# Kernel tuning notes

Hardware: AMD Instinct MI355X
Metric: run time of the kernel (lower is better)

## Reference

```python
import jax, jax.numpy as jnp
import numpy as np

N_GEN, N_LOAD, N_OR, N_EX = 10000, 20000, 35000, 35000
N = N_GEN + N_LOAD + N_OR + N_EX  # 100000 objects
E = 1_600_000                      # edges (avg degree 16)
H = 64                             # N_node_hidden
L_HID = 7                          # N_GCN_layers - 1
NEG = 0.1                          # LeakyReLU negative slope
WS = 0.05                          # weight scale


def setup_inputs() -> dict:
    key = jax.random.key(0)
    ks = jax.random.split(key, 32)
    f = lambda i, s: jax.random.normal(ks[i], s, jnp.float32)
    p = lambda i, s: WS * jax.random.normal(ks[i], s, jnp.float32)
    return {
        "x_gen": f(0, (N_GEN, 3)),
        "x_load": f(1, (N_LOAD, 3)),
        "x_or": f(2, (N_OR, 6)),
        "x_ex": f(3, (N_EX, 6)),
        "edge_index": jax.random.randint(ks[4], (2, E), 0, N, jnp.int32),
        "object_ptv": jnp.arange(N, dtype=jnp.int32),
        "W_gen1": p(5, (3, H)), "b_gen1": p(6, (H,)),
        "W_gen2": p(7, (H, H)), "b_gen2": p(8, (H,)),
        "W_load1": p(9, (3, H)), "b_load1": p(10, (H,)),
        "W_load2": p(11, (H, H)), "b_load2": p(12, (H,)),
        "W_or1": p(13, (6, H)), "b_or1": p(14, (H,)),
        "W_or2": p(15, (H, H)), "b_or2": p(16, (H,)),
        "W_ex1": p(17, (6, H)), "b_ex1": p(18, (H,)),
        "W_ex2": p(19, (H, H)), "b_ex2": p(20, (H,)),
        "Wl_h": p(21, (L_HID, H, H)),
        "Wr_h": p(22, (L_HID, H, H)),
        "b_h": p(23, (L_HID, H)),
        "Wl_last": p(24, (H, 1)),
        "Wr_last": p(25, (H, 1)),
        "b_last": p(26, (1,)),
    }


def _encode(x, W1, b1, W2, b2):
    h = jax.nn.leaky_relu(x @ W1 + b1, NEG)
    return jax.nn.leaky_relu(h @ W2 + b2, NEG)


def reference(x_gen, x_load, x_or, x_ex, edge_index, object_ptv,
              W_gen1, b_gen1, W_gen2, b_gen2,
              W_load1, b_load1, W_load2, b_load2,
              W_or1, b_or1, W_or2, b_or2,
              W_ex1, b_ex1, W_ex2, b_ex2,
              Wl_h, Wr_h, b_h, Wl_last, Wr_last, b_last):
    # per-object-type MLP encoders
    xg = _encode(x_gen, W_gen1, b_gen1, W_gen2, b_gen2)
    xl = _encode(x_load, W_load1, b_load1, W_load2, b_load2)
    xo = _encode(x_or, W_or1, b_or1, W_or2, b_or2)
    xe = _encode(x_ex, W_ex1, b_ex1, W_ex2, b_ex2)
    x = jnp.concatenate([xg, xl, xo, xe], axis=0)[object_ptv]  # [N, H]

    src, dst = edge_index[0], edge_index[1]

    def sage(h, Wl, Wr, b):
        # SAGEConv(aggr='add', root_weight=True): lin_l(sum_j h_j) + lin_r(h_i) + b
        agg = jax.ops.segment_sum(h[src], dst, num_segments=N)  # gather + scatter-add
        return agg @ Wl + h @ Wr + b

    def step(h, params):
        Wl, Wr, b = params
        return jax.nn.leaky_relu(sage(h, Wl, Wr, b), NEG), None

    x, _ = jax.lax.scan(step, x, (Wl_h, Wr_h, b_h))
    return jax.nn.sigmoid(sage(x, Wl_last, Wr_last, b_last))  # [N, 1]
```

## Files before the change

### kernel.cpp

```cpp
#include <hip/hip_runtime.h>
#include <math.h>

#define HD 64
#define NEGS 0.1f
#define CHUNK 2048
#define NPART 8
#define QMAX 440.0f
#define QEPS 1e-30f

typedef unsigned int u32;
typedef unsigned char u8;
typedef float f32x2 __attribute__((ext_vector_type(2)));

__device__ __forceinline__ float leaky(float v) { return v > 0.f ? v : NEGS * v; }

__device__ __forceinline__ u32 pk4(float a, float b, float c, float d) {
    u32 r = __builtin_amdgcn_cvt_pk_fp8_f32(a, b, 0, false);
    r = __builtin_amdgcn_cvt_pk_fp8_f32(c, d, r, true);
    return r;
}

__global__ void zero_i32(int* __restrict__ p, int n) {
    int i = blockIdx.x * blockDim.x + threadIdx.x;
    int stride = gridDim.x * blockDim.x;
    for (; i < n; i += stride) p[i] = 0;
}

template <int IN>
__global__ void encode_k(const float* __restrict__ x,
                         const float* __restrict__ W1, const float* __restrict__ b1,
                         const float* __restrict__ W2, const float* __restrict__ b2,
                         u8* __restrict__ out, float* __restrict__ outS, int n) {
    __shared__ float sW2[HD * HD];
    for (int idx = threadIdx.x; idx < HD * HD; idx += blockDim.x) sW2[idx] = W2[idx];
    __syncthreads();
    int wave = threadIdx.x >> 6, lane = threadIdx.x & 63;
    int i = blockIdx.x * 4 + wave;
    if (i >= n) return;
    float h1 = b1[lane];
#pragma unroll
    for (int d = 0; d < IN; ++d) h1 += x[i * IN + d] * W1[d * HD + lane];
    h1 = leaky(h1);
    float h2 = b2[lane];
#pragma unroll
    for (int k = 0; k < HD; ++k) {
        float hk = __shfl(h1, k);
        h2 += hk * sW2[k * HD + lane];
    }
    float val = leaky(h2);
    float am = fabsf(val);
#pragma unroll
    for (int off = 32; off > 0; off >>= 1) am = fmaxf(am, __shfl_xor(am, off));
    float qs, recip;
    if (am < QEPS) { qs = 0.f; recip = 0.f; }
    else { qs = QMAX / am; recip = am / QMAX; }
    float sv = val * qs;
    float v1 = __shfl_down(sv, 1);
    float v2 = __shfl_down(sv, 2);
    float v3 = __shfl_down(sv, 3);
    if ((lane & 3) == 0)
        ((u32*)(out + (size_t)i * HD))[lane >> 2] = pk4(sv, v1, v2, v3);
    if (lane == 0) outS[i] = recip;
}

__global__ void gather_f8(const u8* __restrict__ enc, const float* __restrict__ encS,
                          const int* __restrict__ ptv,
                          u8* __restrict__ out, float* __restrict__ outS, int n) {
    int idx = blockIdx.x * blockDim.x + threadIdx.x;
    int stride = gridDim.x * blockDim.x;
    int total = n * 4;
    for (; idx < total; idx += stride) {
        int i = idx >> 2, ch = idx & 3;
        int p = ptv[i];
        ((uint4*)(out + (size_t)i * HD))[ch] =
            ((const uint4*)(enc + (size_t)p * HD))[ch];
        if (ch == 0) outS[i] = encS[p];
    }
}

__global__ void __launch_bounds__(256) hist_part(const int* __restrict__ dst,
                                                 int* __restrict__ counts,
                                                 int E_, int part_sz) {
    int part = blockIdx.x & (NPART - 1);
    int slice = blockIdx.x >> 3;
    int nslices = gridDim.x >> 3;
    int lo = part * part_sz, hi = lo + part_sz;
    for (int e = slice * blockDim.x + threadIdx.x; e < E_; e += nslices * blockDim.x) {
        int d = dst[e];
        if (d >= lo && d < hi) atomicAdd(&counts[d], 1);
    }
}

__global__ void scan1(const int* __restrict__ counts, int* __restrict__ bsum, int n) {
    __shared__ int s[256];
    int b = blockIdx.x, t = threadIdx.x;
    int base = b * CHUNK + t * 8;
    int sum = 0;
#pragma unroll
    for (int u = 0; u < 8; ++u) {
        int i = base + u;
        if (i < n) sum += counts[i];
    }
    s[t] = sum;
    __syncthreads();
    for (int off = 128; off > 0; off >>= 1) {
        if (t < off) s[t] += s[t + off];
        __syncthreads();
    }
    if (t == 0) bsum[b] = s[0];
}

__global__ void scan2(int* __restrict__ bsum, int nb, int* __restrict__ row_ptr, int n) {
    if (threadIdx.x == 0 && blockIdx.x == 0) {
        int run = 0;
        for (int b = 0; b < nb; ++b) {
            int v = bsum[b];
            bsum[b] = run;
            run += v;
        }
        row_ptr[n] = run;
    }
}

__global__ void scan3(const int* __restrict__ counts, const int* __restrict__ bsum,
                      int* __restrict__ row_ptr, int* __restrict__ pos, int n) {
    __shared__ int s[256];
    int b = blockIdx.x, t = threadIdx.x;
    int base = b * CHUNK + t * 8;
    int c[8];
    int sum = 0;
#pragma unroll
    for (int u = 0; u < 8; ++u) {
        int i = base + u;
        c[u] = (i < n) ? counts[i] : 0;
        sum += c[u];
    }
    s[t] = sum;
    __syncthreads();
    for (int off = 1; off < 256; off <<= 1) {
        int v = (t >= off) ? s[t - off] : 0;
        __syncthreads();
        s[t] += v;
        __syncthreads();
    }
    int run = bsum[b] + s[t] - sum;
#pragma unroll
    for (int u = 0; u < 8; ++u) {
        int i = base + u;
        if (i < n) {
            row_ptr[i] = run;
            pos[i] = run;
            run += c[u];
        }
    }
}

__global__ void __launch_bounds__(256) scatter_part(const int* __restrict__ src,
                                                    const int* __restrict__ dst,
                                                    int* __restrict__ pos,
                                                    int* __restrict__ col,
                                                    int E_, int part_sz) {
    int part = blockIdx.x & (NPART - 1);
    int slice = blockIdx.x >> 3;
    int nslices = gridDim.x >> 3;
    int lo = part * part_sz, hi = lo + part_sz;
    for (int e = slice * blockDim.x + threadIdx.x; e < E_; e += nslices * blockDim.x) {
        int d = dst[e];
        if (d >= lo && d < hi) {
            int p = atomicAdd(&pos[d], 1);
            col[p] = src[e];
        }
    }
}

__global__ void __launch_bounds__(256) agg_f8(const u8* __restrict__ hin,
                                              const float* __restrict__ hs,
                                              u8* __restrict__ agg,
                                              float* __restrict__ aggS,
                                              const int* __restrict__ row_ptr,
                                              const int* __restrict__ col, int n) {
    int wid = threadIdx.x >> 6, lane = threadIdx.x & 63;
    int g = lane >> 4, s = lane & 15;
    int wpb = blockDim.x >> 6;
    int stride = gridDim.x * wpb;
    for (int i = blockIdx.x * wpb + wid; i < n; i += stride) {
        int beg = row_ptr[i], end = row_ptr[i + 1];
        int deg = end - beg;
        float4 a0 = make_float4(0.f, 0.f, 0.f, 0.f);
        float4 a1 = make_float4(0.f, 0.f, 0.f, 0.f);
        float4 a2 = make_float4(0.f, 0.f, 0.f, 0.f);
        float4 a3 = make_float4(0.f, 0.f, 0.f, 0.f);
        for (int base = 0; base < deg; base += 64) {
            int m = deg - base;
            if (m > 64) m = 64;
            int cidx = (lane < m) ? col[beg + base + lane] : 0;
            int k = g;
            for (; k + 12 < m; k += 16) {
                int c0 = __shfl(cidx, k);
                int c1 = __shfl(cidx, k + 4);
                int c2 = __shfl(cidx, k + 8);
                int c3 = __shfl(cidx, k + 12);
                u32 v0 = ((const u32*)(hin + (size_t)c0 * HD))[s];
                u32 v1 = ((const u32*)(hin + (size_t)c1 * HD))[s];
                u32 v2 = ((const u32*)(hin + (size_t)c2 * HD))[s];
                u32 v3 = ((const u32*)(hin + (size_t)c3 * HD))[s];
                float s0 = hs[c0], s1 = hs[c1], s2 = hs[c2], s3 = hs[c3];
                f32x2 p0 = __builtin_amdgcn_cvt_pk_f32_fp8(v0, false);
                f32x2 q0 = __builtin_amdgcn_cvt_pk_f32_fp8(v0, true);
                f32x2 p1 = __builtin_amdgcn_cvt_pk_f32_fp8(v1, false);
                f32x2 q1 = __builtin_amdgcn_cvt_pk_f32_fp8(v1, true);
                f32x2 p2 = __builtin_amdgcn_cvt_pk_f32_fp8(v2, false);
                f32x2 q2 = __builtin_amdgcn_cvt_pk_f32_fp8(v2, true);
                f32x2 p3 = __builtin_amdgcn_cvt_pk_f32_fp8(v3, false);
                f32x2 q3 = __builtin_amdgcn_cvt_pk_f32_fp8(v3, true);
                a0.x = fmaf(p0.x, s0, a0.x); a0.y = fmaf(p0.y, s0, a0.y);
                a0.z = fmaf(q0.x, s0, a0.z); a0.w = fmaf(q0.y, s0, a0.w);
                a1.x = fmaf(p1.x, s1, a1.x); a1.y = fmaf(p1.y, s1, a1.y);
                a1.z = fmaf(q1.x, s1, a1.z); a1.w = fmaf(q1.y, s1, a1.w);
                a2.x = fmaf(p2.x, s2, a2.x); a2.y = fmaf(p2.y, s2, a2.y);
                a2.z = fmaf(q2.x, s2, a2.z); a2.w = fmaf(q2.y, s2, a2.w);
                a3.x = fmaf(p3.x, s3, a3.x); a3.y = fmaf(p3.y, s3, a3.y);
                a3.z = fmaf(q3.x, s3, a3.z); a3.w = fmaf(q3.y, s3, a3.w);
            }
            for (; k < m; k += 4) {
                int c0 = __shfl(cidx, k);
                u32 v0 = ((const u32*)(hin + (size_t)c0 * HD))[s];
                float s0 = hs[c0];
                f32x2 p0 = __builtin_amdgcn_cvt_pk_f32_fp8(v0, false);
                f32x2 q0 = __builtin_amdgcn_cvt_pk_f32_fp8(v0, true);
                a0.x = fmaf(p0.x, s0, a0.x); a0.y = fmaf(p0.y, s0, a0.y);
                a0.z = fmaf(q0.x, s0, a0.z); a0.w = fmaf(q0.y, s0, a0.w);
            }
        }
        a0.x += a1.x + a2.x + a3.x;
        a0.y += a1.y + a2.y + a3.y;
        a0.z += a1.z + a2.z + a3.z;
        a0.w += a1.w + a2.w + a3.w;
        a0.x += __shfl_xor(a0.x, 16);
        a0.y += __shfl_xor(a0.y, 16);
        a0.z += __shfl_xor(a0.z, 16);
        a0.w += __shfl_xor(a0.w, 16);
        a0.x += __shfl_xor(a0.x, 32);
        a0.y += __shfl_xor(a0.y, 32);
        a0.z += __shfl_xor(a0.z, 32);
        a0.w += __shfl_xor(a0.w, 32);
        float am = fmaxf(fmaxf(fabsf(a0.x), fabsf(a0.y)),
                         fmaxf(fabsf(a0.z), fabsf(a0.w)));
        am = fmaxf(am, __shfl_xor(am, 1));
        am = fmaxf(am, __shfl_xor(am, 2));
        am = fmaxf(am, __shfl_xor(am, 4));
        am = fmaxf(am, __shfl_xor(am, 8));
        float qs, recip;
        if (am < QEPS) { qs = 0.f; recip = 0.f; }
        else { qs = QMAX / am; recip = am / QMAX; }
        if (g == 0) {
            ((u32*)(agg + (size_t)i * HD))[s] =
                pk4(a0.x * qs, a0.y * qs, a0.z * qs, a0.w * qs);
            if (s == 0) aggS[i] = recip;
        }
    }
}

__global__ void __launch_bounds__(256) sage_gemm_f8(const u8* __restrict__ agg,
                                                    const float* __restrict__ aggS,
                                                    const u8* __restrict__ h,
                                                    const float* __restrict__ hS,
                                                    u8* __restrict__ hout,
                                                    float* __restrict__ houtS,
                                                    const float* __restrict__ Wl,
                                                    const float* __restrict__ Wr,
                                                    const float* __restrict__ bias, int n) {
    __shared__ float Ws[128][64];
    __shared__ float Xs[64][132];
    int tid = threadIdx.x;
    for (int idx = tid; idx < 64 * 64; idx += 256) {
        int k = idx >> 6, j = idx & 63;
        Ws[k][j] = Wl[idx];
        Ws[64 + k][j] = Wr[idx];
    }
    int tcol = tid & 15, trow = tid >> 4;
    int j0 = tcol * 4;
    float b0 = bias[j0], b1 = bias[j0 + 1], b2 = bias[j0 + 2], b3 = bias[j0 + 3];
    int ntiles = (n + 63) >> 6;
    for (int t = blockIdx.x; t < ntiles; t += gridDim.x) {
        int base = t << 6;
        __syncthreads();
#pragma unroll
        for (int u = 0; u < 4; ++u) {
            int idx = tid + u * 256;
            int row = idx >> 4, ch = idx & 15;
            int grow = base + row;
            uint2 q = make_uint2(0u, 0u);
            float sc = 0.f;
            if (grow < n) {
                q = (ch < 8) ? ((const uint2*)(agg + (size_t)grow * HD))[ch]
                             : ((const uint2*)(h + (size_t)grow * HD))[ch - 8];
                sc = (ch < 8) ? aggS[grow] : hS[grow];
            }
            f32x2 p0 = __builtin_amdgcn_cvt_pk_f32_fp8(q.x, false);
            f32x2 p1 = __builtin_amdgcn_cvt_pk_f32_fp8(q.x, true);
            f32x2 p2 = __builtin_amdgcn_cvt_pk_f32_fp8(q.y, false);
            f32x2 p3 = __builtin_amdgcn_cvt_pk_f32_fp8(q.y, true);
            float* xp = &Xs[row][ch * 8];
            xp[0] = p0.x * sc; xp[1] = p0.y * sc; xp[2] = p1.x * sc; xp[3] = p1.y * sc;
            xp[4] = p2.x * sc; xp[5] = p2.y * sc; xp[6] = p3.x * sc; xp[7] = p3.y * sc;
        }
        __syncthreads();
        float acc[4][4];
#pragma unroll
        for (int r = 0; r < 4; ++r)
#pragma unroll
            for (int c = 0; c < 4; ++c) acc[r][c] = 0.f;
#pragma unroll 4
        for (int k4 = 0; k4 < 32; ++k4) {
            int k = k4 * 4;
            float4 x0 = *(const float4*)&Xs[trow][k];
            float4 x1 = *(const float4*)&Xs[trow + 16][k];
            float4 x2 = *(const float4*)&Xs[trow + 32][k];
            float4 x3 = *(const float4*)&Xs[trow + 48][k];
            float4 w0 = *(const float4*)&Ws[k][j0];
            float4 w1 = *(const float4*)&Ws[k + 1][j0];
            float4 w2 = *(const float4*)&Ws[k + 2][j0];
            float4 w3 = *(const float4*)&Ws[k + 3][j0];
            float4 xr[4] = {x0, x1, x2, x3};
#pragma unroll
            for (int r = 0; r < 4; ++r) {
                acc[r][0] += xr[r].x * w0.x + xr[r].y * w1.x + xr[r].z * w2.x + xr[r].w * w3.x;
                acc[r][1] += xr[r].x * w0.y + xr[r].y * w1.y + xr[r].z * w2.y + xr[r].w * w3.y;
                acc[r][2] += xr[r].x * w0.z + xr[r].y * w1.z + xr[r].z * w2.z + xr[r].w * w3.z;
                acc[r][3] += xr[r].x * w0.w + xr[r].y * w1.w + xr[r].z * w2.w + xr[r].w * w3.w;
            }
        }
#pragma unroll
        for (int r = 0; r < 4; ++r) {
            int grow = base + trow + 16 * r;
            float o0 = leaky(acc[r][0] + b0);
            float o1 = leaky(acc[r][1] + b1);
            float o2 = leaky(acc[r][2] + b2);
            float o3 = leaky(acc[r][3] + b3);
            float am = fmaxf(fmaxf(fabsf(o0), fabsf(o1)), fmaxf(fabsf(o2), fabsf(o3)));
            am = fmaxf(am, __shfl_xor(am, 1));
            am = fmaxf(am, __shfl_xor(am, 2));
            am = fmaxf(am, __shfl_xor(am, 4));
            am = fmaxf(am, __shfl_xor(am, 8));
            float qs, recip;
            if (am < QEPS) { qs = 0.f; recip = 0.f; }
            else { qs = QMAX / am; recip = am / QMAX; }
            if (grow < n) {
                ((u32*)(hout + (size_t)grow * HD))[tcol] =
                    pk4(o0 * qs, o1 * qs, o2 * qs, o3 * qs);
                if (tcol == 0) houtS[grow] = recip;
            }
        }
    }
}

__global__ void __launch_bounds__(256) dot_f8(const u8* __restrict__ h,
                                              const float* __restrict__ hS,
                                              const float* __restrict__ Wl,
                                              const float* __restrict__ Wr,
                                              float* __restrict__ sb, float* __restrict__ tb,
                                              int n) {
    int wid = threadIdx.x >> 6, lane = threadIdx.x & 63;
    float wl = Wl[lane], wr = Wr[lane];
    int wpb = blockDim.x >> 6;
    int stride = gridDim.x * wpb;
    for (int i = blockIdx.x * wpb + wid; i < n; i += stride) {
        u32 v = ((const u32*)(h + (size_t)i * HD))[lane >> 2];
        float sc = hS[i];
        f32x2 lo = __builtin_amdgcn_cvt_pk_f32_fp8(v, false);
        f32x2 hi = __builtin_amdgcn_cvt_pk_f32_fp8(v, true);
        float hv = ((lane & 2) ? ((lane & 1) ? hi.y : hi.x)
                               : ((lane & 1) ? lo.y : lo.x)) * sc;
        float a = hv * wl;
        float c = hv * wr;
#pragma unroll
        for (int off = 32; off > 0; off >>= 1) {
            a += __shfl_xor(a, off);
            c += __shfl_xor(c, off);
        }
        if (lane == 0) {
            sb[i] = a;
            tb[i] = c;
        }
    }
}

__global__ void __launch_bounds__(256) last_k(const float* __restrict__ sb,
                                              const float* __restrict__ tb,
                                              const int* __restrict__ row_ptr,
                                              const int* __restrict__ col,
                                              const float* __restrict__ b_last,
                                              float* __restrict__ out, int n) {
    float b0 = b_last[0];
    int stride = gridDim.x * blockDim.x;
    for (int i = blockIdx.x * blockDim.x + threadIdx.x; i < n; i += stride) {
        int beg = row_ptr[i], end = row_ptr[i + 1];
        float acc = 0.f;
        for (int k = beg; k < end; ++k) acc += sb[col[k]];
        out[i] = 1.f / (1.f + expf(-(acc + tb[i] + b0)));
    }
}

extern "C" void kernel_launch(void* const* d_in, const int* in_sizes, int n_in,
                              void* d_out, int out_size, void* d_ws, size_t ws_size,
                              hipStream_t stream) {
    const float* x_gen = (const float*)d_in[0];
    const float* x_load = (const float*)d_in[1];
    const float* x_or = (const float*)d_in[2];
    const float* x_ex = (const float*)d_in[3];
    const int* edge = (const int*)d_in[4];
    const int* ptv = (const int*)d_in[5];
    const float* W_gen1 = (const float*)d_in[6];
    const float* b_gen1 = (const float*)d_in[7];
    const float* W_gen2 = (const float*)d_in[8];
    const float* b_gen2 = (const float*)d_in[9];
    const float* W_load1 = (const float*)d_in[10];
    const float* b_load1 = (const float*)d_in[11];
    const float* W_load2 = (const float*)d_in[12];
    const float* b_load2 = (const float*)d_in[13];
    const float* W_or1 = (const float*)d_in[14];
    const float* b_or1 = (const float*)d_in[15];
    const float* W_or2 = (const float*)d_in[16];
    const float* b_or2 = (const float*)d_in[17];
    const float* W_ex1 = (const float*)d_in[18];
    const float* b_ex1 = (const float*)d_in[19];
    const float* W_ex2 = (const float*)d_in[20];
    const float* b_ex2 = (const float*)d_in[21];
    const float* Wl_h = (const float*)d_in[22];
    const float* Wr_h = (const float*)d_in[23];
    const float* b_h = (const float*)d_in[24];
    const float* Wl_last = (const float*)d_in[25];
    const float* Wr_last = (const float*)d_in[26];
    const float* b_last = (const float*)d_in[27];

    int n_gen = in_sizes[0] / 3;
    int n_load = in_sizes[1] / 3;
    int n_or = in_sizes[2] / 6;
    int n_ex = in_sizes[3] / 6;
    int E_ = in_sizes[4] / 2;
    int N_ = in_sizes[5];
    const int* srcv = edge;
    const int* dstv = edge + E_;

    char* ws = (char*)d_ws;
    size_t off = 0;
    auto alloc = [&](size_t bytes) -> void* {
        void* p = ws + off;
        off = (off + bytes + 255) & ~(size_t)255;
        return p;
    };
    u8* enc = (u8*)alloc((size_t)N_ * HD);
    float* encS = (float*)alloc((size_t)N_ * 4);
    u8* hA = (u8*)alloc((size_t)N_ * HD);
    float* sA = (float*)alloc((size_t)N_ * 4);
    u8* hB = (u8*)alloc((size_t)N_ * HD);
    float* sB = (float*)alloc((size_t)N_ * 4);
    int* counts = (int*)alloc((size_t)N_ * 4);
    int* row_ptr = (int*)alloc((size_t)(N_ + 1) * 4);
    int* pos = (int*)alloc((size_t)N_ * 4);
    int* bsum = (int*)alloc(256 * 4);
    int* csr_col = (int*)alloc((size_t)E_ * 4);
    float* sbuf = (float*)alloc((size_t)N_ * 4);
    float* tbuf = (float*)alloc((size_t)N_ * 4);
    u8* agg = enc;
    float* aggS = encS;
    (void)ws_size;

    int part_sz = (N_ + NPART - 1) / NPART;

    zero_i32<<<256, 256, 0, stream>>>(counts, N_);

    encode_k<3><<<(n_gen + 3) / 4, 256, 0, stream>>>(x_gen, W_gen1, b_gen1, W_gen2, b_gen2,
                                                     enc, encS, n_gen);
    encode_k<3><<<(n_load + 3) / 4, 256, 0, stream>>>(x_load, W_load1, b_load1, W_load2, b_load2,
                                                      enc + (size_t)n_gen * HD, encS + n_gen, n_load);
    encode_k<6><<<(n_or + 3) / 4, 256, 0, stream>>>(x_or, W_or1, b_or1, W_or2, b_or2,
                                                    enc + (size_t)(n_gen + n_load) * HD,
                                                    encS + n_gen + n_load, n_or);
    encode_k<6><<<(n_ex + 3) / 4, 256, 0, stream>>>(x_ex, W_ex1, b_ex1, W_ex2, b_ex2,
                                                    enc + (size_t)(n_gen + n_load + n_or) * HD,
                                                    encS + n_gen + n_load + n_or, n_ex);

    gather_f8<<<512, 256, 0, stream>>>(enc, encS, ptv, hA, sA, N_);

    hist_part<<<2048, 256, 0, stream>>>(dstv, counts, E_, part_sz);
    int nb = (N_ + CHUNK - 1) / CHUNK;
    scan1<<<nb, 256, 0, stream>>>(counts, bsum, N_);
    scan2<<<1, 64, 0, stream>>>(bsum, nb, row_ptr, N_);
    scan3<<<nb, 256, 0, stream>>>(counts, bsum, row_ptr, pos, N_);
    scatter_part<<<2048, 256, 0, stream>>>(srcv, dstv, pos, csr_col, E_, part_sz);

    int ntiles = (N_ + 63) >> 6;
    int ggrid = ntiles < 512 ? ntiles : 512;
    u8* cur = hA;   float* curS = sA;
    u8* nxt = hB;   float* nxtS = sB;
    for (int l = 0; l < 7; ++l) {
        agg_f8<<<4096, 256, 0, stream>>>(cur, curS, agg, aggS, row_ptr, csr_col, N_);
        sage_gemm_f8<<<ggrid, 256, 0, stream>>>(agg, aggS, cur, curS, nxt, nxtS,
                                                Wl_h + (size_t)l * HD * HD,
                                                Wr_h + (size_t)l * HD * HD,
                                                b_h + (size_t)l * HD, N_);
        u8* t = cur; cur = nxt; nxt = t;
        float* ts = curS; curS = nxtS; nxtS = ts;
    }
    dot_f8<<<1024, 256, 0, stream>>>(cur, curS, Wl_last, Wr_last, sbuf, tbuf, N_);
    last_k<<<512, 256, 0, stream>>>(sbuf, tbuf, row_ptr, csr_col, b_last,
                                    (float*)d_out, N_);
}
```

Baseline: 830.2 us.

## Assign one node per 16-lane group in fp8 aggregation kernel

The aggregation kernel now maps each destination node to a 16-lane quarter-wave group instead of a full 64-lane wavefront. Each group loads up to 16 neighbour indices at a time and walks its neighbours serially, which removes the cross-group shuffle reductions and the idle store lanes. With average degree 16, the old layout left most of each wavefront's lanes doing little work. The launch grid is resized to cover about 16 nodes per block. The tradeoff is lower memory-level parallelism per node, and more divergence when degrees differ between groups in the same wave.

```diff
diff --git a/kernel.cpp b/kernel.cpp
--- a/kernel.cpp
+++ b/kernel.cpp
@@ -179,32 +179,34 @@
                                               float* __restrict__ aggS,
                                               const int* __restrict__ row_ptr,
                                               const int* __restrict__ col, int n) {
-    int wid = threadIdx.x >> 6, lane = threadIdx.x & 63;
-    int g = lane >> 4, s = lane & 15;
-    int wpb = blockDim.x >> 6;
-    int stride = gridDim.x * wpb;
-    for (int i = blockIdx.x * wpb + wid; i < n; i += stride) {
+    int tid = threadIdx.x;
+    int g = (tid >> 4) & 3;
+    int s = tid & 15;
+    int gid = (blockIdx.x * blockDim.x + tid) >> 4;
+    int ngroups = (gridDim.x * blockDim.x) >> 4;
+    int gbase = g << 4;
+    for (int i = gid; i < n; i += ngroups) {
         int beg = row_ptr[i], end = row_ptr[i + 1];
         int deg = end - beg;
         float4 a0 = make_float4(0.f, 0.f, 0.f, 0.f);
         float4 a1 = make_float4(0.f, 0.f, 0.f, 0.f);
         float4 a2 = make_float4(0.f, 0.f, 0.f, 0.f);
         float4 a3 = make_float4(0.f, 0.f, 0.f, 0.f);
-        for (int base = 0; base < deg; base += 64) {
+        for (int base = 0; base < deg; base += 16) {
             int m = deg - base;
-            if (m > 64) m = 64;
-            int cidx = (lane < m) ? col[beg + base + lane] : 0;
-            int k = g;
-            for (; k + 12 < m; k += 16) {
-                int c0 = __shfl(cidx, k);
-                int c1 = __shfl(cidx, k + 4);
-                int c2 = __shfl(cidx, k + 8);
-                int c3 = __shfl(cidx, k + 12);
-                u32 v0 = ((const u32*)(hin + (size_t)c0 * HD))[s];
-                u32 v1 = ((const u32*)(hin + (size_t)c1 * HD))[s];
-                u32 v2 = ((const u32*)(hin + (size_t)c2 * HD))[s];
-                u32 v3 = ((const u32*)(hin + (size_t)c3 * HD))[s];
-                float s0 = hs[c0], s1 = hs[c1], s2 = hs[c2], s3 = hs[c3];
+            if (m > 16) m = 16;
+            int cidx = (s < m) ? col[beg + base + s] : 0;
+            int k = 0;
+            for (; k + 3 < m; k += 4) {
+                int r0 = __shfl(cidx, gbase + k);
+                int r1 = __shfl(cidx, gbase + k + 1);
+                int r2 = __shfl(cidx, gbase + k + 2);
+                int r3 = __shfl(cidx, gbase + k + 3);
+                u32 v0 = ((const u32*)(hin + (size_t)r0 * HD))[s];
+                u32 v1 = ((const u32*)(hin + (size_t)r1 * HD))[s];
+                u32 v2 = ((const u32*)(hin + (size_t)r2 * HD))[s];
+                u32 v3 = ((const u32*)(hin + (size_t)r3 * HD))[s];
+                float s0 = hs[r0], s1 = hs[r1], s2 = hs[r2], s3 = hs[r3];
                 f32x2 p0 = __builtin_amdgcn_cvt_pk_f32_fp8(v0, false);
                 f32x2 q0 = __builtin_amdgcn_cvt_pk_f32_fp8(v0, true);
                 f32x2 p1 = __builtin_amdgcn_cvt_pk_f32_fp8(v1, false);
@@ -222,10 +224,10 @@
                 a3.x = fmaf(p3.x, s3, a3.x); a3.y = fmaf(p3.y, s3, a3.y);
                 a3.z = fmaf(q3.x, s3, a3.z); a3.w = fmaf(q3.y, s3, a3.w);
             }
-            for (; k < m; k += 4) {
-                int c0 = __shfl(cidx, k);
-                u32 v0 = ((const u32*)(hin + (size_t)c0 * HD))[s];
-                float s0 = hs[c0];
+            for (; k < m; ++k) {
+                int r0 = __shfl(cidx, gbase + k);
+                u32 v0 = ((const u32*)(hin + (size_t)r0 * HD))[s];
+                float s0 = hs[r0];
                 f32x2 p0 = __builtin_amdgcn_cvt_pk_f32_fp8(v0, false);
                 f32x2 q0 = __builtin_amdgcn_cvt_pk_f32_fp8(v0, true);
                 a0.x = fmaf(p0.x, s0, a0.x); a0.y = fmaf(p0.y, s0, a0.y);
@@ -236,14 +238,6 @@
         a0.y += a1.y + a2.y + a3.y;
         a0.z += a1.z + a2.z + a3.z;
         a0.w += a1.w + a2.w + a3.w;
-        a0.x += __shfl_xor(a0.x, 16);
-        a0.y += __shfl_xor(a0.y, 16);
-        a0.z += __shfl_xor(a0.z, 16);
-        a0.w += __shfl_xor(a0.w, 16);
-        a0.x += __shfl_xor(a0.x, 32);
-        a0.y += __shfl_xor(a0.y, 32);
-        a0.z += __shfl_xor(a0.z, 32);
-        a0.w += __shfl_xor(a0.w, 32);
         float am = fmaxf(fmaxf(fabsf(a0.x), fabsf(a0.y)),
                          fmaxf(fabsf(a0.z), fabsf(a0.w)));
         am = fmaxf(am, __shfl_xor(am, 1));
@@ -253,11 +247,9 @@
         float qs, recip;
         if (am < QEPS) { qs = 0.f; recip = 0.f; }
         else { qs = QMAX / am; recip = am / QMAX; }
-        if (g == 0) {
-            ((u32*)(agg + (size_t)i * HD))[s] =
-                pk4(a0.x * qs, a0.y * qs, a0.z * qs, a0.w * qs);
-            if (s == 0) aggS[i] = recip;
-        }
+        ((u32*)(agg + (size_t)i * HD))[s] =
+            pk4(a0.x * qs, a0.y * qs, a0.z * qs, a0.w * qs);
+        if (s == 0) aggS[i] = recip;
     }
 }
 
@@ -493,10 +485,12 @@
 
     int ntiles = (N_ + 63) >> 6;
     int ggrid = ntiles < 512 ? ntiles : 512;
+    int agrid = (N_ + 15) / 16;
+    if (agrid > 6250) agrid = 6250;
     u8* cur = hA;   float* curS = sA;
     u8* nxt = hB;   float* nxtS = sB;
     for (int l = 0; l < 7; ++l) {
-        agg_f8<<<4096, 256, 0, stream>>>(cur, curS, agg, aggS, row_ptr, csr_col, N_);
+        agg_f8<<<agrid, 256, 0, stream>>>(cur, curS, agg, aggS, row_ptr, csr_col, N_);
         sage_gemm_f8<<<ggrid, 256, 0, stream>>>(agg, aggS, cur, curS, nxt, nxtS,
                                                 Wl_h + (size_t)l * HD * HD,
                                                 Wr_h + (size_t)l * HD * HD,
```

New measurement: 767.0 us. 1.08x faster.
